# Performance work log

Hardware: AMD Instinct MI355X
Metric: run time of the kernel (lower is better)

Reference implementation:

```python
import math
import jax, jax.numpy as jnp
import numpy as np

NQ = 4   # n_qubits
NL = 2   # n_layers
H = 16   # num_heads


def _apply_gate(state, gate, q, batched):
    """Apply a 1-qubit gate on wire q to batched state [N, 2**NQ]."""
    n = state.shape[0]
    left, right = 2 ** q, 2 ** (NQ - 1 - q)
    s = state.reshape(n, left, 2, right)
    eq = 'nab,nlbr->nlar' if batched else 'ab,nlbr->nlar'
    return jnp.einsum(eq, gate, s).reshape(n, 2 ** NQ)


def _rot(phi, theta, omega):
    """PennyLane Rot(phi, theta, omega) = RZ(omega) RY(theta) RZ(phi), 2x2 unitary."""
    c = jnp.cos(theta / 2).astype(jnp.complex64)
    s = jnp.sin(theta / 2).astype(jnp.complex64)
    ep = jnp.exp(-0.5j * (phi + omega).astype(jnp.complex64))
    em = jnp.exp(0.5j * (phi - omega).astype(jnp.complex64))
    m00 = ep * c
    m01 = -em * s
    m10 = jnp.conj(em) * s
    m11 = jnp.conj(ep) * c
    return jnp.stack([jnp.stack([m00, m01]), jnp.stack([m10, m11])])


def _cnot01(state):
    """CNOT with control wire 0, target wire 1 on [N, 16]."""
    n = state.shape[0]
    s = state.reshape(n, 2, 2, 2 ** (NQ - 2))
    s = jnp.stack([s[:, 0], s[:, 1, ::-1]], axis=1)
    return s.reshape(n, 2 ** NQ)


def _quantum_block(inputs, params):
    """Analytic state-vector simulation of the PennyLane circuit.

    inputs: [N, NQ] rotation angles (AngleEmbedding, default RX).
    params: [NL, NQ, 3] Rot parameters.
    Returns [N, NQ] Pauli-Z expectation values.
    """
    n = inputs.shape[0]
    state = jnp.zeros((n, 2 ** NQ), jnp.complex64).at[:, 0].set(1.0)
    # AngleEmbedding: RX(inputs[:, q]) on wire q
    for q in range(NQ):
        a = inputs[:, q] * 0.5
        c = jnp.cos(a).astype(jnp.complex64)
        s = (-1j) * jnp.sin(a).astype(jnp.complex64)
        gate = jnp.stack([jnp.stack([c, s], -1), jnp.stack([s, c], -1)], -2)  # [N,2,2]
        state = _apply_gate(state, gate, q, batched=True)
    # Variational layers
    for l in range(NL):
        for q in range(NQ):
            g = _rot(params[l, q, 0], params[l, q, 1], params[l, q, 2])
            state = _apply_gate(state, g, q, batched=False)
        state = _cnot01(state)
    probs = (jnp.abs(state) ** 2).reshape(n, 2, 2, 2, 2)
    z = jnp.array([1.0, -1.0], probs.dtype)
    letters = 'abcd'
    evs = [jnp.einsum(f'nabcd,{letters[i]}->n', probs, z) for i in range(NQ)]
    return jnp.stack(evs, axis=-1)


def reference(x, params, w_q, w_k, w_v, w_o):
    B, S, E = x.shape
    dk = E // H

    def proj(w):
        return (x @ w.T).reshape(B, S, H, dk).transpose(0, 2, 1, 3)  # [B,H,S,dk]

    q, k, v = proj(w_q), proj(w_k), proj(w_v)

    def inject(t):
        ang = t[..., :NQ].reshape(-1, NQ)
        ev = _quantum_block(ang, params).reshape(B, H, S, NQ).astype(t.dtype)
        return t.at[..., :NQ].set(ev)

    q, k, v = inject(q), inject(k), inject(v)
    scores = jnp.einsum('bhqd,bhkd->bhqk', q, k) / math.sqrt(dk)
    attn = jax.nn.softmax(scores, axis=-1)
    out = jnp.einsum('bhqk,bhkd->bhqd', attn, v)
    out = out.transpose(0, 2, 1, 3).reshape(B, S, E)
    return out @ w_o.T


def setup_inputs() -> dict:
    key = jax.random.key(0)
    ks = jax.random.split(key, 6)
    B, S, E = 2, 2048, 1024
    scale = 1.0 / math.sqrt(E)
    return {
        'x': jax.random.normal(ks[0], (B, S, E), jnp.float32),
        'params': jax.random.normal(ks[1], (NL, NQ, 3), jnp.float32),
        'w_q': jax.random.normal(ks[2], (E, E), jnp.float32) * scale,
        'w_k': jax.random.normal(ks[3], (E, E), jnp.float32) * scale,
        'w_v': jax.random.normal(ks[4], (E, E), jnp.float32) * scale,
        'w_o': jax.random.normal(ks[5], (E, E), jnp.float32) * scale,
    }
```

## Files before the change

kernel.cpp:

```cpp
#include <hip/hip_runtime.h>
#include <math.h>

#define BATCH 2
#define S_LEN 2048
#define E_DIM 1024
#define NHEAD 16
#define DK 64
#define NROWS (BATCH * S_LEN)

#define SM_A    0.18033688011f
#define SM_INVA 5.5451774444795623f
#define SM_B   -4.32808512267f

typedef _Float16 f16x8 __attribute__((ext_vector_type(8)));
typedef _Float16 f16x4 __attribute__((ext_vector_type(4)));
typedef float    f32x4 __attribute__((ext_vector_type(4)));

__device__ __forceinline__ void glds16(_Float16* lds, const _Float16* g) {
    __builtin_amdgcn_global_load_lds(
        (const __attribute__((address_space(1))) unsigned int*)g,
        (__attribute__((address_space(3))) unsigned int*)lds,
        16, 0, 0);
}

__global__ __launch_bounds__(256) void conv_all(
    const float* __restrict__ x,  const float* __restrict__ wq,
    const float* __restrict__ wk, const float* __restrict__ wv,
    const float* __restrict__ wo,
    _Float16* __restrict__ xh,  _Float16* __restrict__ wqh,
    _Float16* __restrict__ wkh, _Float16* __restrict__ wvh,
    _Float16* __restrict__ woh) {
    const int id = blockIdx.x;
    const float* src; _Float16* dst; int lid;
    if (id < 4096)      { src = x;  dst = xh;  lid = id; }
    else if (id < 5120) { src = wq; dst = wqh; lid = id - 4096; }
    else if (id < 6144) { src = wk; dst = wkh; lid = id - 5120; }
    else if (id < 7168) { src = wv; dst = wvh; lid = id - 6144; }
    else                { src = wo; dst = woh; lid = id - 7168; }
    const int i = lid * 256 + threadIdx.x;
    float4 v = ((const float4*)src)[i];
    f16x4 h;
    h[0] = (_Float16)v.x; h[1] = (_Float16)v.y;
    h[2] = (_Float16)v.z; h[3] = (_Float16)v.w;
    ((f16x4*)dst)[i] = h;
}

__device__ __forceinline__ void gemm_body32(const _Float16* __restrict__ X,
                                            const _Float16* __restrict__ W,
                                            void* __restrict__ dstv, int mode,
                                            float oscale, _Float16* smem) {
    const int tid  = threadIdx.x;
    const int lane = tid & 63;
    const int w    = tid >> 6;
    const int wy = w >> 1, wx = w & 1;
    const int l15 = lane & 15, quad = lane >> 4;
    const int sw3 = l15 & 3;
    const int m0 = blockIdx.y * 128, c0 = blockIdx.x * 128;

    const int lrow = lane >> 2;
    const int gcol = ((lane & 3) ^ (lrow & 3)) * 8;
    const _Float16* xg = X + (size_t)(m0 + w * 32 + lrow) * E_DIM + gcol;
    const _Float16* wg = W + (size_t)(c0 + w * 32 + lrow) * E_DIM + gcol;
    const int woff = (w * 32) * 32;

    f32x4 acc[4][4];
#pragma unroll
    for (int i = 0; i < 4; ++i)
#pragma unroll
        for (int j = 0; j < 4; ++j) acc[i][j] = 0.f;

    glds16(smem + woff,              xg);
    glds16(smem + woff + 512,        xg + (size_t)16 * E_DIM);
    glds16(smem + 4096 + woff,       wg);
    glds16(smem + 4096 + woff + 512, wg + (size_t)16 * E_DIM);
    __syncthreads();

    for (int t = 0; t < E_DIM / 32; ++t) {
        const int buf = t & 1;
        _Float16* Xs = smem + buf * 8192;
        _Float16* Ws = Xs + 4096;
        if (t < E_DIM / 32 - 1) {
            _Float16* Xn = smem + (buf ^ 1) * 8192;
            const int k0 = (t + 1) * 32;
            glds16(Xn + woff,              xg + k0);
            glds16(Xn + woff + 512,        xg + (size_t)16 * E_DIM + k0);
            glds16(Xn + 4096 + woff,       wg + k0);
            glds16(Xn + 4096 + woff + 512, wg + (size_t)16 * E_DIM + k0);
        }

        f16x8 af[4], bf[4];
        const int pc = (quad ^ sw3) * 8;
#pragma unroll
        for (int i = 0; i < 4; ++i)
            af[i] = *(const f16x8*)&Xs[(wy * 64 + i * 16 + l15) * 32 + pc];
#pragma unroll
        for (int j = 0; j < 4; ++j)
            bf[j] = *(const f16x8*)&Ws[(wx * 64 + j * 16 + l15) * 32 + pc];
#pragma unroll
        for (int i = 0; i < 4; ++i)
#pragma unroll
            for (int j = 0; j < 4; ++j)
                acc[i][j] = __builtin_amdgcn_mfma_f32_16x16x32_f16(af[i], bf[j], acc[i][j], 0, 0, 0);

        __syncthreads();
    }

    if (mode == 2) {
        _Float16* Ct = smem;
        const int b  = m0 >> 11;
        const int s0 = m0 & 2047;
#pragma unroll
        for (int hph = 0; hph < 2; ++hph) {
            if (wx == hph) {
#pragma unroll
                for (int i = 0; i < 4; ++i)
#pragma unroll
                    for (int j = 0; j < 4; ++j) {
                        const int col_l = j * 16 + l15;
                        const int rowb  = wy * 64 + i * 16 + quad * 4;
                        f16x4 pk;
#pragma unroll
                        for (int r = 0; r < 4; ++r) pk[r] = (_Float16)(acc[i][j][r] * oscale);
                        *(f16x4*)&Ct[col_l * 136 + rowb] = pk;
                    }
            }
            __syncthreads();
#pragma unroll
            for (int it = 0; it < 4; ++it) {
                const int c     = it * 256 + tid;
                const int col_l = c >> 4;
                const int rc    = c & 15;
                f16x8 v = *(const f16x8*)&Ct[col_l * 136 + rc * 8];
                const int e = c0 + hph * 64 + col_l, h = e >> 6, d = e & 63;
                *(f16x8*)((_Float16*)dstv + ((size_t)((b * NHEAD + h) * DK + d)) * S_LEN + s0 + rc * 8) = v;
            }
            __syncthreads();
        }
        return;
    }

#pragma unroll
    for (int i = 0; i < 4; ++i)
#pragma unroll
        for (int j = 0; j < 4; ++j)
#pragma unroll
            for (int r = 0; r < 4; ++r) {
                const int row = m0 + wy * 64 + i * 16 + quad * 4 + r;
                const int col = c0 + wx * 64 + j * 16 + l15;
                const int b = row >> 11, s = row & 2047;
                const int h = col >> 6,  d = col & 63;
                ((_Float16*)dstv)[(((size_t)(b * NHEAD + h) * S_LEN + s) * DK) + d] =
                    (_Float16)(acc[i][j][r] * oscale);
            }
}

__global__ __launch_bounds__(256, 4) void gemm_qkv(
    const _Float16* __restrict__ X,
    const _Float16* __restrict__ WQ, const _Float16* __restrict__ WK,
    const _Float16* __restrict__ WV,
    _Float16* __restrict__ Qh, _Float16* __restrict__ Kh,
    _Float16* __restrict__ VTh) {
    __shared__ __align__(16) _Float16 smem[2 * 8192];
    const int z = blockIdx.z;
    const _Float16* W = (z == 0) ? WQ : (z == 1) ? WK : WV;
    void* dst = (z == 0) ? (void*)Qh : (z == 1) ? (void*)Kh : (void*)VTh;
    const float osc = (z == 1) ? SM_A : 1.0f;
    gemm_body32(X, W, dst, (z == 2) ? 2 : 1, osc, smem);
}

__global__ __launch_bounds__(256, 3) void gemm_out2(const _Float16* __restrict__ X,
                                                    const _Float16* __restrict__ W,
                                                    float* __restrict__ dst) {
    __shared__ __align__(16) _Float16 smem[2 * 12288];

    const int tid  = threadIdx.x;
    const int lane = tid & 63;
    const int w    = tid >> 6;
    const int wy = w >> 1, wx = w & 1;
    const int l15 = lane & 15, quad = lane >> 4;
    const int sw  = l15 & 7;
    const int m0 = blockIdx.y * 128, c0 = blockIdx.x * 64;

    const int lrow = lane >> 3;
    const int gcol = ((lane & 7) ^ lrow) * 8;
    const _Float16* xg = X + (size_t)(m0 + w * 32 + lrow) * E_DIM + gcol;
    const _Float16* wg = W + (size_t)(c0 + w * 16 + lrow) * E_DIM + gcol;
    const int xoff = (w * 32) * 64;
    const int woff = (w * 16) * 64;

    f32x4 acc[4][2];
#pragma unroll
    for (int i = 0; i < 4; ++i)
#pragma unroll
        for (int j = 0; j < 2; ++j) acc[i][j] = 0.f;

#pragma unroll
    for (int c = 0; c < 4; ++c)
        glds16(smem + xoff + c * 512, xg + (size_t)c * 8 * E_DIM);
#pragma unroll
    for (int c = 0; c < 2; ++c)
        glds16(smem + 8192 + woff + c * 512, wg + (size_t)c * 8 * E_DIM);
    __syncthreads();

    for (int t = 0; t < E_DIM / 64; ++t) {
        const int buf = t & 1;
        _Float16* Xs = smem + buf * 12288;
        _Float16* Ws = Xs + 8192;
        if (t < E_DIM / 64 - 1) {
            _Float16* Xn = smem + (buf ^ 1) * 12288;
            const int k0 = (t + 1) * 64;
#pragma unroll
            for (int c = 0; c < 4; ++c)
                glds16(Xn + xoff + c * 512, xg + (size_t)c * 8 * E_DIM + k0);
#pragma unroll
            for (int c = 0; c < 2; ++c)
                glds16(Xn + 8192 + woff + c * 512, wg + (size_t)c * 8 * E_DIM + k0);
        }

#pragma unroll
        for (int ks = 0; ks < 2; ++ks) {
            f16x8 af[4], bf[2];
#pragma unroll
            for (int i = 0; i < 4; ++i) {
                const int pc = ((ks * 4 + quad) ^ sw) * 8;
                af[i] = *(const f16x8*)&Xs[(wy * 64 + i * 16 + l15) * 64 + pc];
            }
#pragma unroll
            for (int j = 0; j < 2; ++j) {
                const int pc = ((ks * 4 + quad) ^ sw) * 8;
                bf[j] = *(const f16x8*)&Ws[(wx * 32 + j * 16 + l15) * 64 + pc];
            }
#pragma unroll
            for (int i = 0; i < 4; ++i)
#pragma unroll
                for (int j = 0; j < 2; ++j)
                    acc[i][j] = __builtin_amdgcn_mfma_f32_16x16x32_f16(af[i], bf[j], acc[i][j], 0, 0, 0);
        }
        __syncthreads();
    }

#pragma unroll
    for (int i = 0; i < 4; ++i)
#pragma unroll
        for (int j = 0; j < 2; ++j)
#pragma unroll
            for (int r = 0; r < 4; ++r) {
                const int row = m0 + wy * 64 + i * 16 + quad * 4 + r;
                const int col = c0 + wx * 32 + j * 16 + l15;
                dst[(size_t)row * E_DIM + col] = acc[i][j][r];
            }
}

__device__ __forceinline__ void apply_gate(float ar[16], float ai[16], int stride,
                                           float g00r, float g00i, float g01r, float g01i,
                                           float g10r, float g10i, float g11r, float g11i) {
#pragma unroll
    for (int i0 = 0; i0 < 16; ++i0) {
        if (i0 & stride) continue;
        const int i1 = i0 + stride;
        const float s0r = ar[i0], s0i = ai[i0];
        const float s1r = ar[i1], s1i = ai[i1];
        ar[i0] = g00r * s0r - g00i * s0i + g01r * s1r - g01i * s1i;
        ai[i0] = g00r * s0i + g00i * s0r + g01r * s1i + g01i * s1r;
        ar[i1] = g10r * s0r - g10i * s0i + g11r * s1r - g11i * s1i;
        ai[i1] = g10r * s0i + g10i * s0r + g11r * s1i + g11i * s1r;
    }
}

__global__ __launch_bounds__(256) void quantum_inject(_Float16* __restrict__ Q,
                                                      _Float16* __restrict__ K,
                                                      _Float16* __restrict__ VT,
                                                      const float* __restrict__ params) {
    const int id = blockIdx.x * 256 + threadIdx.x;
    const int which = id >> 16;
    const int rem = id & 65535;

    float angv[4];
    _Float16* qkbase = nullptr;
    _Float16* vbase  = nullptr;
    if (which == 2) {
        const int bh = rem >> 11, s = rem & 2047;
        vbase = VT + ((size_t)bh * DK) * S_LEN + s;
#pragma unroll
        for (int d = 0; d < 4; ++d) angv[d] = (float)vbase[(size_t)d * S_LEN];
    } else {
        qkbase = (which == 0 ? Q : K) + (size_t)rem * DK;
        const f16x4 a4 = *(const f16x4*)qkbase;
        const float asc = (which == 1) ? SM_INVA : 1.0f;
#pragma unroll
        for (int d = 0; d < 4; ++d) angv[d] = (float)a4[d] * asc;
    }

    float ar[16], ai[16];
#pragma unroll
    for (int i = 0; i < 16; ++i) { ar[i] = 0.f; ai[i] = 0.f; }
    ar[0] = 1.f;

#pragma unroll
    for (int q = 0; q < 4; ++q) {
        float sh, ch;
        sincosf(0.5f * angv[q], &sh, &ch);
        apply_gate(ar, ai, 8 >> q, ch, 0.f, 0.f, -sh, 0.f, -sh, ch, 0.f);
    }

#pragma unroll
    for (int l = 0; l < 2; ++l) {
#pragma unroll
        for (int q = 0; q < 4; ++q) {
            const float* pp = params + (l * 4 + q) * 3;
            const float phi = pp[0], th = pp[1], om = pp[2];
            float st, ct, sa, ca, sb, cb;
            sincosf(0.5f * th, &st, &ct);
            sincosf(0.5f * (phi + om), &sa, &ca);
            sincosf(0.5f * (phi - om), &sb, &cb);
            apply_gate(ar, ai, 8 >> q,
                       ct * ca, -ct * sa,
                       -st * cb, -st * sb,
                       st * cb, -st * sb,
                       ct * ca, ct * sa);
        }
#pragma unroll
        for (int r = 0; r < 4; ++r) {
            float tr = ar[8 + r], ti = ai[8 + r];
            ar[8 + r] = ar[12 + r]; ai[8 + r] = ai[12 + r];
            ar[12 + r] = tr;        ai[12 + r] = ti;
        }
    }

    float ev[4] = {0.f, 0.f, 0.f, 0.f};
#pragma unroll
    for (int i = 0; i < 16; ++i) {
        const float p = ar[i] * ar[i] + ai[i] * ai[i];
        ev[0] += (i & 8) ? -p : p;
        ev[1] += (i & 4) ? -p : p;
        ev[2] += (i & 2) ? -p : p;
        ev[3] += (i & 1) ? -p : p;
    }
    if (which == 2) {
#pragma unroll
        for (int d = 0; d < 4; ++d) vbase[(size_t)d * S_LEN] = (_Float16)ev[d];
    } else {
        const float osc = (which == 1) ? SM_A : 1.0f;
        f16x4 o;
#pragma unroll
        for (int d = 0; d < 4; ++d) o[d] = (_Float16)(ev[d] * osc);
        *(f16x4*)qkbase = o;
    }
}

__global__ __launch_bounds__(256, 3) void attn10(const _Float16* __restrict__ Q,
                                                 const _Float16* __restrict__ K,
                                                 const _Float16* __restrict__ VT,
                                                 _Float16* __restrict__ ctx) {
    __shared__ __align__(16) _Float16 KVs[3][2][64 * 64];

    const int tid = threadIdx.x, lane = tid & 63, w = tid >> 6;
    const int l15 = lane & 15, quad = lane >> 4;
    const int sw  = l15 & 7;
    const int bh = blockIdx.y;
    const int qbase = blockIdx.x * 128 + w * 32;

    const _Float16* Qb = Q  + (size_t)bh * S_LEN * DK;
    const _Float16* Kb = K  + (size_t)bh * S_LEN * DK;
    const _Float16* Vb = VT + (size_t)bh * DK * S_LEN;

    const int lrow = lane >> 3;
    const int gcol = ((lane & 7) ^ lrow) * 8;
    const int sr0  = 32 * (w >> 1) + 8 * (lrow >> 2) + 4 * (w & 1) + (lrow & 3);
    const _Float16* kg = Kb + (size_t)sr0 * DK + gcol;
    const _Float16* vg = Vb + (size_t)(w * 16 + lrow) * S_LEN + gcol;

    auto stage = [&](int u, int bidx) {
        const int kt = u * 64;
        _Float16* kb = &KVs[bidx][0][(w * 16) * 64];
        _Float16* vb = &KVs[bidx][1][(w * 16) * 64];
        glds16(kb,       kg + (size_t)kt * DK);
        glds16(kb + 512, kg + (size_t)(kt + 16) * DK);
        glds16(vb,       vg + (size_t)kt);
        glds16(vb + 512, vg + (size_t)8 * S_LEN + kt);
    };

    f16x8 bf[2][2];
#pragma unroll
    for (int qn = 0; qn < 2; ++qn)
#pragma unroll
        for (int ks = 0; ks < 2; ++ks)
            bf[qn][ks] = *(const f16x8*)(Qb + (size_t)(qbase + qn * 16 + l15) * DK + ks * 32 + quad * 8);

    f32x4 oacc[4][2];
#pragma unroll
    for (int dt = 0; dt < 4; ++dt)
#pragma unroll
        for (int qn = 0; qn < 2; ++qn) oacc[dt][qn] = 0.f;
    float lpart[2] = {0.f, 0.f};

    stage(0, 0);
    stage(1, 1);
    asm volatile("s_waitcnt vmcnt(4)" ::: "memory");
    __builtin_amdgcn_s_barrier();

    int buf = 0, nbuf = 2;
    for (int t = 0; t < S_LEN / 64; ++t) {
        if (t < S_LEN / 64 - 2) stage(t + 2, nbuf);

        f16x8 af[4][2], vt[4][2];
#pragma unroll
        for (int kc = 0; kc < 4; ++kc)
#pragma unroll
            for (int ks = 0; ks < 2; ++ks)
                af[kc][ks] = *(const f16x8*)&KVs[buf][0][(kc * 16 + l15) * 64 + ((ks * 4 + quad) ^ sw) * 8];
#pragma unroll
        for (int dt = 0; dt < 4; ++dt)
#pragma unroll
            for (int kh = 0; kh < 2; ++kh)
                vt[dt][kh] = *(const f16x8*)&KVs[buf][1][(dt * 16 + l15) * 64 + ((kh * 4 + quad) ^ sw) * 8];

        f16x4 pk4s[4][2];
#pragma unroll
        for (int kc = 0; kc < 4; ++kc)
#pragma unroll
            for (int qn = 0; qn < 2; ++qn) {
                f32x4 st = SM_B;
                st = __builtin_amdgcn_mfma_f32_16x16x32_f16(af[kc][0], bf[qn][0], st, 0, 0, 0);
                st = __builtin_amdgcn_mfma_f32_16x16x32_f16(af[kc][1], bf[qn][1], st, 0, 0, 0);
                float ps = 0.f;
                f16x4 pk;
#pragma unroll
                for (int r = 0; r < 4; ++r) {
                    const float p = __builtin_amdgcn_exp2f(st[r]);
                    ps += p;
                    pk[r] = (_Float16)p;
                }
                lpart[qn] += ps;
                pk4s[kc][qn] = pk;
            }

#pragma unroll
        for (int dt = 0; dt < 4; ++dt)
#pragma unroll
            for (int qn = 0; qn < 2; ++qn)
#pragma unroll
                for (int kh = 0; kh < 2; ++kh) {
                    const f16x8 pb = __builtin_shufflevector(
                        pk4s[2 * kh][qn], pk4s[2 * kh + 1][qn],
                        0, 1, 2, 3, 4, 5, 6, 7);
                    oacc[dt][qn] = __builtin_amdgcn_mfma_f32_16x16x32_f16(
                        vt[dt][kh], pb, oacc[dt][qn], 0, 0, 0);
                }

        if (t < S_LEN / 64 - 2) {
            asm volatile("s_waitcnt vmcnt(4)" ::: "memory");
        } else if (t == S_LEN / 64 - 2) {
            asm volatile("s_waitcnt vmcnt(0)" ::: "memory");
        }
        __builtin_amdgcn_s_barrier();

        buf  = (buf == 2)  ? 0 : buf + 1;
        nbuf = (nbuf == 2) ? 0 : nbuf + 1;
    }

    float inv[2];
#pragma unroll
    for (int qn = 0; qn < 2; ++qn) {
        float l = lpart[qn];
        l += __shfl_xor(l, 16);
        l += __shfl_xor(l, 32);
        inv[qn] = 1.f / l;
    }

    _Float16* ep = &KVs[0][0][0] + w * (32 * 72);
#pragma unroll
    for (int dt = 0; dt < 4; ++dt)
#pragma unroll
        for (int qn = 0; qn < 2; ++qn) {
            f16x4 ov;
#pragma unroll
            for (int r = 0; r < 4; ++r) ov[r] = (_Float16)(oacc[dt][qn][r] * inv[qn]);
            *(f16x4*)&ep[(qn * 16 + l15) * 72 + dt * 16 + quad * 4] = ov;
        }

    const int b = bh >> 4, h = bh & 15;
#pragma unroll
    for (int i = 0; i < 4; ++i) {
        const int c = i * 64 + lane;
        const int row = c >> 3, c8 = c & 7;
        f16x8 v = *(const f16x8*)&ep[row * 72 + c8 * 8];
        *(f16x8*)(ctx + (size_t)(b * S_LEN + qbase + row) * E_DIM + h * DK + c8 * 8) = v;
    }
}

extern "C" void kernel_launch(void* const* d_in, const int* in_sizes, int n_in,
                              void* d_out, int out_size, void* d_ws, size_t ws_size,
                              hipStream_t stream) {
    const float* x      = (const float*)d_in[0];
    const float* params = (const float*)d_in[1];
    const float* w_q    = (const float*)d_in[2];
    const float* w_k    = (const float*)d_in[3];
    const float* w_v    = (const float*)d_in[4];
    const float* w_o    = (const float*)d_in[5];
    float* out = (float*)d_out;

    const size_t TENS = (size_t)NROWS * E_DIM;
    const size_t WEL  = (size_t)E_DIM * E_DIM;
    _Float16* xh  = (_Float16*)d_ws;
    _Float16* wqh = xh  + TENS;
    _Float16* wkh = wqh + WEL;
    _Float16* wvh = wkh + WEL;
    _Float16* woh = wvh + WEL;
    _Float16* Qh  = woh + WEL;
    _Float16* Kh  = Qh  + TENS;
    _Float16* VTh = Kh  + TENS;
    _Float16* CTXh= VTh + TENS;

    dim3 blk(256);

    conv_all<<<dim3(8192), blk, 0, stream>>>(x, w_q, w_k, w_v, w_o,
                                             xh, wqh, wkh, wvh, woh);

    gemm_qkv<<<dim3(E_DIM / 128, NROWS / 128, 3), blk, 0, stream>>>(
        xh, wqh, wkh, wvh, Qh, Kh, VTh);

    quantum_inject<<<dim3(768), blk, 0, stream>>>(Qh, Kh, VTh, params);

    attn10<<<dim3(S_LEN / 128, BATCH * NHEAD), blk, 0, stream>>>(Qh, Kh, VTh, CTXh);

    gemm_out2<<<dim3(E_DIM / 64, NROWS / 128), blk, 0, stream>>>(CTXh, woh, out);
}
```

Baseline: 185.3 us.

## Triple-buffer QKV GEMM LDS pipeline with two tiles in flight

Converts the QKV projection GEMM main loop from double to triple LDS buffering, issuing global-to-LDS loads two k-tiles ahead. It replaces __syncthreads with explicit vmcnt waits plus s_barrier so the next tile's loads can stay outstanding across the barrier. The goal is to hide more global memory latency. In exchange, LDS use rises by half and launch bounds drop from 4 to 3 blocks per CU, which may reduce occupancy.

```diff
diff --git a/kernel.cpp b/kernel.cpp
--- a/kernel.cpp
+++ b/kernel.cpp
@@ -63,31 +63,32 @@
     const _Float16* wg = W + (size_t)(c0 + w * 32 + lrow) * E_DIM + gcol;
     const int woff = (w * 32) * 32;
 
+    auto stage = [&](int u, int bidx) {
+        _Float16* base = smem + bidx * 8192;
+        const int k0 = u * 32;
+        glds16(base + woff,              xg + k0);
+        glds16(base + woff + 512,        xg + (size_t)16 * E_DIM + k0);
+        glds16(base + 4096 + woff,       wg + k0);
+        glds16(base + 4096 + woff + 512, wg + (size_t)16 * E_DIM + k0);
+    };
+
     f32x4 acc[4][4];
 #pragma unroll
     for (int i = 0; i < 4; ++i)
 #pragma unroll
         for (int j = 0; j < 4; ++j) acc[i][j] = 0.f;
 
-    glds16(smem + woff,              xg);
-    glds16(smem + woff + 512,        xg + (size_t)16 * E_DIM);
-    glds16(smem + 4096 + woff,       wg);
-    glds16(smem + 4096 + woff + 512, wg + (size_t)16 * E_DIM);
-    __syncthreads();
-
+    stage(0, 0);
+    stage(1, 1);
+    asm volatile("s_waitcnt vmcnt(4)" ::: "memory");
+    __builtin_amdgcn_s_barrier();
+
+    int buf = 0, nbuf = 2;
     for (int t = 0; t < E_DIM / 32; ++t) {
-        const int buf = t & 1;
+        if (t < E_DIM / 32 - 2) stage(t + 2, nbuf);
+
         _Float16* Xs = smem + buf * 8192;
         _Float16* Ws = Xs + 4096;
-        if (t < E_DIM / 32 - 1) {
-            _Float16* Xn = smem + (buf ^ 1) * 8192;
-            const int k0 = (t + 1) * 32;
-            glds16(Xn + woff,              xg + k0);
-            glds16(Xn + woff + 512,        xg + (size_t)16 * E_DIM + k0);
-            glds16(Xn + 4096 + woff,       wg + k0);
-            glds16(Xn + 4096 + woff + 512, wg + (size_t)16 * E_DIM + k0);
-        }
-
         f16x8 af[4], bf[4];
         const int pc = (quad ^ sw3) * 8;
 #pragma unroll
@@ -102,7 +103,15 @@
             for (int j = 0; j < 4; ++j)
                 acc[i][j] = __builtin_amdgcn_mfma_f32_16x16x32_f16(af[i], bf[j], acc[i][j], 0, 0, 0);
 
-        __syncthreads();
+        if (t < E_DIM / 32 - 2) {
+            asm volatile("s_waitcnt vmcnt(4)" ::: "memory");
+        } else if (t == E_DIM / 32 - 2) {
+            asm volatile("s_waitcnt vmcnt(0)" ::: "memory");
+        }
+        __builtin_amdgcn_s_barrier();
+
+        buf  = (buf == 2)  ? 0 : buf + 1;
+        nbuf = (nbuf == 2) ? 0 : nbuf + 1;
     }
 
     if (mode == 2) {
@@ -154,13 +163,13 @@
             }
 }
 
-__global__ __launch_bounds__(256, 4) void gemm_qkv(
+__global__ __launch_bounds__(256, 3) void gemm_qkv(
     const _Float16* __restrict__ X,
     const _Float16* __restrict__ WQ, const _Float16* __restrict__ WK,
     const _Float16* __restrict__ WV,
     _Float16* __restrict__ Qh, _Float16* __restrict__ Kh,
     _Float16* __restrict__ VTh) {
-    __shared__ __align__(16) _Float16 smem[2 * 8192];
+    __shared__ __align__(16) _Float16 smem[3 * 8192];
     const int z = blockIdx.z;
     const _Float16* W = (z == 0) ? WQ : (z == 1) ? WK : WV;
     void* dst = (z == 0) ? (void*)Qh : (z == 1) ? (void*)Kh : (void*)VTh;
```

After: 190.6 us. 2.9% more time.
